# Performance work log

Hardware: AMD Instinct MI355X
Metric: run time of the kernel (lower is better)

## Reference

```python
import jax, jax.numpy as jnp
import numpy as np

S = 2048          # sequence length == max_seq_len
B = 256           # input_bits per token
H = 8             # num voting heads
NPER = 12         # RAM bits per neuron: min(similarity_bits, 12)
NPOS = 11         # relative-position bits: ceil(log2(max_seq_len))
SIM = 2 * B + NPOS  # similarity input bits = [query | key | rel_dist]
THRESH = H // 2   # threshold aggregation cutoff
MAXD = S - 1


def setup_inputs() -> dict:
    key = jax.random.key(0)
    k1, k2, k3 = jax.random.split(key, 3)
    tokens = jax.random.randint(k1, (S, B), 0, 2).astype(jnp.int32)      # bit tokens
    conn = jax.random.randint(k2, (H, NPER), 0, SIM).astype(jnp.int32)   # RAM wiring per head
    table = jax.random.randint(k3, (H, 2 ** NPER), 0, 2).astype(jnp.int32)  # RAM contents (0/1)
    return {"tokens": tokens, "conn": conn, "table": table}


def reference(tokens, conn, table):
    powers = (1 << jnp.arange(NPER)).astype(jnp.int32)            # address bit weights
    q_mask = (conn < B).astype(jnp.int32)
    k_mask = ((conn >= B) & (conn < 2 * B)).astype(jnp.int32)
    p_mask = (conn >= 2 * B).astype(jnp.int32)

    # Address decomposes additively over the three concat regions since wiring is fixed.
    tq = jnp.take(tokens, jnp.clip(conn, 0, B - 1), axis=1)        # [S,H,NPER]
    q_contrib = jnp.sum(tq * (q_mask * powers)[None], axis=-1)     # [S,H]
    tk = jnp.take(tokens, jnp.clip(conn - B, 0, B - 1), axis=1)
    k_contrib = jnp.sum(tk * (k_mask * powers)[None], axis=-1)     # [S,H]

    d = jnp.arange(S)
    rel_bits = ((d[:, None] >> jnp.arange(NPOS)[None, :]) & 1).astype(jnp.int32)  # [S,NPOS]
    tp = jnp.take(rel_bits, jnp.clip(conn - 2 * B, 0, NPOS - 1), axis=1)          # [S,H,NPER]
    p_contrib = jnp.sum(tp * (p_mask * powers)[None], axis=-1)     # [S,H] indexed by distance

    i = jnp.arange(S)
    dist = jnp.clip(i[:, None] - i[None, :], 0, MAXD)              # [S,S]
    addr = q_contrib[:, None, :] + k_contrib[None, :, :] + p_contrib[dist]  # [S,S,H]
    head_bits = table[jnp.arange(H)[None, None, :], addr]          # [S,S,H] RAM lookups

    causal = i[None, :] <= i[:, None]
    votes = jnp.where(causal, head_bits.sum(-1), 0)                # [S,S]

    # threshold aggregation: XOR (per-bit parity) of tokens with vote >= THRESH
    include = (votes >= THRESH).astype(jnp.int32)                  # [S,S]
    parity = jnp.einsum('ij,jb->ib', include, tokens) % 2          # [S,B]
    # fallback: first token achieving the max vote when nothing clears threshold
    fallback = tokens[jnp.argmax(votes, axis=1)]                   # [S,B]
    any_included = include.sum(axis=1, keepdims=True) > 0
    out = jnp.where(any_included, parity, fallback)
    return out.astype(jnp.uint8)
```

## Files before the change

kernel.cpp:

```cpp
#include <hip/hip_runtime.h>
#include <stdint.h>

#define S 2048
#define B 256
#define H 8
#define NPER 12
#define NPOS 11
#define THRESH 4

typedef unsigned long long u64;
typedef uint32_t u32;


__global__ void prep_kernel(const int* __restrict__ tokens,
                            const int* __restrict__ conn,
                            const int* __restrict__ table,
                            u64* __restrict__ packed_tokens,
                            uint16_t* __restrict__ qc,
                            uint16_t* __restrict__ kc,
                            uint16_t* __restrict__ pc,
                            u64* __restrict__ ptab) {
    const int bi = blockIdx.x;
    const int tid = threadIdx.x;

    if (bi >= S) {
        int k = (bi - S) * 256 + tid;
        int h = k >> 6, w = k & 63;
        const int* src = table + h * 4096 + w * 64;
        u64 v = 0;
        #pragma unroll 8
        for (int b = 0; b < 64; ++b) v |= (u64)(src[b] & 1) << b;
        ptab[k] = v;
        return;
    }

    __shared__ u64 srow[4];
    const int i = bi;
    const int lane = tid & 63, wave = tid >> 6;

    int t = tokens[i * B + tid];
    u64 m = __ballot(t != 0);
    if (lane == 0) {
        srow[wave] = m;
        packed_tokens[i * 4 + wave] = m;
    }
    __syncthreads();

    if (tid < H) {
        int h = tid;
        int q = 0, k = 0, p = 0;
        #pragma unroll
        for (int n = 0; n < NPER; ++n) {
            int c = conn[h * NPER + n];
            if (c < B) {
                q |= (int)((srow[c >> 6] >> (c & 63)) & 1) << n;
            } else if (c < 2 * B) {
                int cc = c - B;
                k |= (int)((srow[cc >> 6] >> (cc & 63)) & 1) << n;
            } else {
                int idx = c - 2 * B;
                p |= ((i >> idx) & 1) << n;
            }
        }
        qc[i * 8 + h] = (uint16_t)q;
        kc[i * 8 + h] = (uint16_t)k;
        pc[i * 8 + h] = (uint16_t)p;
    }
}

__launch_bounds__(256)
__global__ void main_kernel(const u64* __restrict__ packed_tokens,
                            const uint16_t* __restrict__ qc,
                            const uint16_t* __restrict__ kc,
                            const uint16_t* __restrict__ pc,
                            const u64* __restrict__ ptab,
                            int* __restrict__ out) {
    __shared__ u32 s_tab[1024];
    __shared__ u64 s_xor[4][4];
    __shared__ int s_key[4];
    __shared__ int s_any[4];

    const int tid = threadIdx.x;
    const int lane = tid & 63, wave = tid >> 6;

    ((uint4*)s_tab)[tid] = ((const uint4*)ptab)[tid];
    __syncthreads();

    auto do_row = [&](int i) {
        const u64* qv = (const u64*)(qc + i * 8);
        const u64 q0 = qv[0], q1 = qv[1];

        u64 x0 = 0, x1 = 0, x2 = 0, x3 = 0;
        int bestv = -1, bestj = 0, any = 0;

        const int niter = (i + 512) >> 9;
        for (int it = 0; it < niter; ++it) {
            const int ja = tid + (it << 9);
            const int jb = ja + 256;
            const int jca = min(ja, i), jcb = min(jb, i);
            const int da = i - jca, db = i - jcb;

            const ulonglong2 kA = *(const ulonglong2*)(kc + jca * 8);
            const ulonglong2 pA = *(const ulonglong2*)(pc + da * 8);
            const ulonglong2 kB = *(const ulonglong2*)(kc + jcb * 8);
            const ulonglong2 pB = *(const ulonglong2*)(pc + db * 8);
            const ulonglong2 tA0 = *(const ulonglong2*)(packed_tokens + jca * 4);
            const ulonglong2 tA1 = *(const ulonglong2*)(packed_tokens + jca * 4 + 2);
            const ulonglong2 tB0 = *(const ulonglong2*)(packed_tokens + jcb * 4);
            const ulonglong2 tB1 = *(const ulonglong2*)(packed_tokens + jcb * 4 + 2);

            const u64 aa0 = q0 + kA.x + pA.x, aa1 = q1 + kA.y + pA.y;
            const u64 ab0 = q0 + kB.x + pB.x, ab1 = q1 + kB.y + pB.y;

            int vA = 0, vB = 0;
            #pragma unroll
            for (int h = 0; h < 4; ++h) {
                { u32 w = (u32)(aa0 >> (16 * h + 5)) & 127;
                  vA += (int)((s_tab[h * 128 + w] >> ((u32)(aa0 >> (16 * h)) & 31)) & 1); }
                { u32 w = (u32)(aa1 >> (16 * h + 5)) & 127;
                  vA += (int)((s_tab[(h + 4) * 128 + w] >> ((u32)(aa1 >> (16 * h)) & 31)) & 1); }
                { u32 w = (u32)(ab0 >> (16 * h + 5)) & 127;
                  vB += (int)((s_tab[h * 128 + w] >> ((u32)(ab0 >> (16 * h)) & 31)) & 1); }
                { u32 w = (u32)(ab1 >> (16 * h + 5)) & 127;
                  vB += (int)((s_tab[(h + 4) * 128 + w] >> ((u32)(ab1 >> (16 * h)) & 31)) & 1); }
            }

            const bool actA = (ja <= i), actB = (jb <= i);
            const bool incA = actA && (vA >= THRESH);
            const bool incB = actB && (vB >= THRESH);
            const u64 mA = incA ? ~0ull : 0ull;
            const u64 mB = incB ? ~0ull : 0ull;
            x0 ^= (tA0.x & mA) ^ (tB0.x & mB);
            x1 ^= (tA0.y & mA) ^ (tB0.y & mB);
            x2 ^= (tA1.x & mA) ^ (tB1.x & mB);
            x3 ^= (tA1.y & mA) ^ (tB1.y & mB);
            any |= (int)incA | (int)incB;

            const int kvA = actA ? vA : -1;
            const int kvB = actB ? vB : -1;
            if (kvA > bestv) { bestv = kvA; bestj = ja; }
            if (kvB > bestv) { bestv = kvB; bestj = jb; }
        }

        int key = ((bestv + 1) << 16) | (2047 - bestj);
        u64 anym = __ballot(any != 0);
        #pragma unroll
        for (int off = 32; off > 0; off >>= 1) {
            key = max(key, __shfl_xor(key, off));
            x0 ^= __shfl_xor(x0, off);
            x1 ^= __shfl_xor(x1, off);
            x2 ^= __shfl_xor(x2, off);
            x3 ^= __shfl_xor(x3, off);
        }

        if (lane == 0) {
            s_xor[wave][0] = x0; s_xor[wave][1] = x1;
            s_xor[wave][2] = x2; s_xor[wave][3] = x3;
            s_key[wave] = key;
            s_any[wave] = (anym != 0ull) ? 1 : 0;
        }
        __syncthreads();

        const int fk = max(max(s_key[0], s_key[1]), max(s_key[2], s_key[3]));
        const int fa = s_any[0] | s_any[1] | s_any[2] | s_any[3];
        const int widx = tid >> 6, bitb = tid & 63;
        const u64 xw = s_xor[0][widx] ^ s_xor[1][widx] ^ s_xor[2][widx] ^ s_xor[3][widx];
        int o;
        if (fa) {
            o = (int)((xw >> bitb) & 1);
        } else {
            const int bj = 2047 - (fk & 0xFFFF);
            o = (int)((packed_tokens[bj * 4 + widx] >> bitb) & 1);
        }
        out[i * B + tid] = o;
        __syncthreads();
    };

    const int b = blockIdx.x;
    do_row(b);
    do_row(2047 - b);
}

extern "C" void kernel_launch(void* const* d_in, const int* in_sizes, int n_in,
                              void* d_out, int out_size, void* d_ws, size_t ws_size,
                              hipStream_t stream) {
    const int* tokens = (const int*)d_in[0];
    const int* conn   = (const int*)d_in[1];
    const int* table  = (const int*)d_in[2];
    int* out = (int*)d_out;

    uint8_t* ws = (uint8_t*)d_ws;
    u64* packed_tokens = (u64*)(ws);
    uint16_t* qc = (uint16_t*)(ws + 65536);
    uint16_t* kc = (uint16_t*)(ws + 98304);
    uint16_t* pc = (uint16_t*)(ws + 131072);
    u64* ptab    = (u64*)(ws + 163840);

    prep_kernel<<<S + 2, 256, 0, stream>>>(tokens, conn, table,
                                           packed_tokens, qc, kc, pc, ptab);
    main_kernel<<<S / 2, 256, 0, stream>>>(packed_tokens, qc, kc, pc, ptab, out);
}
```

Measured before the change: 22.03 us.

## Fuse paired short and long row processing into one loop sharing key and token loads

Each block handles row b and row 2047-b. Previously it did them one after the other. Now a single loop over the long row's keys also computes the short row whenever the iteration is in range, so the kc and packed-token loads are shared. The two rows' reductions are merged into one shuffle pass and one barrier. The 'any included' ballot is replaced by testing whether the best vote exceeds THRESH, and launch bounds now request 4 blocks per CU. The doubled accumulators raise register pressure, which could conflict with the occupancy hint.

```diff
diff --git a/kernel.cpp b/kernel.cpp
--- a/kernel.cpp
+++ b/kernel.cpp
@@ -68,7 +68,19 @@
     }
 }
 
-__launch_bounds__(256)
+__device__ __forceinline__ int vote8(const u32* s_tab, u64 a0, u64 a1) {
+    int v = 0;
+    #pragma unroll
+    for (int h = 0; h < 4; ++h) {
+        { u32 w = (u32)(a0 >> (16 * h + 5)) & 127;
+          v += (int)((s_tab[h * 128 + w] >> ((u32)(a0 >> (16 * h)) & 31)) & 1); }
+        { u32 w = (u32)(a1 >> (16 * h + 5)) & 127;
+          v += (int)((s_tab[(h + 4) * 128 + w] >> ((u32)(a1 >> (16 * h)) & 31)) & 1); }
+    }
+    return v;
+}
+
+__launch_bounds__(256, 4)
 __global__ void main_kernel(const u64* __restrict__ packed_tokens,
                             const uint16_t* __restrict__ qc,
                             const uint16_t* __restrict__ kc,
@@ -76,9 +88,7 @@
                             const u64* __restrict__ ptab,
                             int* __restrict__ out) {
     __shared__ u32 s_tab[1024];
-    __shared__ u64 s_xor[4][4];
-    __shared__ int s_key[4];
-    __shared__ int s_any[4];
+    __shared__ u64 s_red[4][9];
 
     const int tid = threadIdx.x;
     const int lane = tid & 63, wave = tid >> 6;
@@ -86,99 +96,115 @@
     ((uint4*)s_tab)[tid] = ((const uint4*)ptab)[tid];
     __syncthreads();
 
-    auto do_row = [&](int i) {
-        const u64* qv = (const u64*)(qc + i * 8);
-        const u64 q0 = qv[0], q1 = qv[1];
-
-        u64 x0 = 0, x1 = 0, x2 = 0, x3 = 0;
-        int bestv = -1, bestj = 0, any = 0;
-
-        const int niter = (i + 512) >> 9;
-        for (int it = 0; it < niter; ++it) {
-            const int ja = tid + (it << 9);
-            const int jb = ja + 256;
-            const int jca = min(ja, i), jcb = min(jb, i);
-            const int da = i - jca, db = i - jcb;
-
-            const ulonglong2 kA = *(const ulonglong2*)(kc + jca * 8);
-            const ulonglong2 pA = *(const ulonglong2*)(pc + da * 8);
-            const ulonglong2 kB = *(const ulonglong2*)(kc + jcb * 8);
-            const ulonglong2 pB = *(const ulonglong2*)(pc + db * 8);
-            const ulonglong2 tA0 = *(const ulonglong2*)(packed_tokens + jca * 4);
-            const ulonglong2 tA1 = *(const ulonglong2*)(packed_tokens + jca * 4 + 2);
-            const ulonglong2 tB0 = *(const ulonglong2*)(packed_tokens + jcb * 4);
-            const ulonglong2 tB1 = *(const ulonglong2*)(packed_tokens + jcb * 4 + 2);
-
-            const u64 aa0 = q0 + kA.x + pA.x, aa1 = q1 + kA.y + pA.y;
-            const u64 ab0 = q0 + kB.x + pB.x, ab1 = q1 + kB.y + pB.y;
-
-            int vA = 0, vB = 0;
-            #pragma unroll
-            for (int h = 0; h < 4; ++h) {
-                { u32 w = (u32)(aa0 >> (16 * h + 5)) & 127;
-                  vA += (int)((s_tab[h * 128 + w] >> ((u32)(aa0 >> (16 * h)) & 31)) & 1); }
-                { u32 w = (u32)(aa1 >> (16 * h + 5)) & 127;
-                  vA += (int)((s_tab[(h + 4) * 128 + w] >> ((u32)(aa1 >> (16 * h)) & 31)) & 1); }
-                { u32 w = (u32)(ab0 >> (16 * h + 5)) & 127;
-                  vB += (int)((s_tab[h * 128 + w] >> ((u32)(ab0 >> (16 * h)) & 31)) & 1); }
-                { u32 w = (u32)(ab1 >> (16 * h + 5)) & 127;
-                  vB += (int)((s_tab[(h + 4) * 128 + w] >> ((u32)(ab1 >> (16 * h)) & 31)) & 1); }
-            }
-
-            const bool actA = (ja <= i), actB = (jb <= i);
-            const bool incA = actA && (vA >= THRESH);
-            const bool incB = actB && (vB >= THRESH);
-            const u64 mA = incA ? ~0ull : 0ull;
-            const u64 mB = incB ? ~0ull : 0ull;
-            x0 ^= (tA0.x & mA) ^ (tB0.x & mB);
-            x1 ^= (tA0.y & mA) ^ (tB0.y & mB);
-            x2 ^= (tA1.x & mA) ^ (tB1.x & mB);
-            x3 ^= (tA1.y & mA) ^ (tB1.y & mB);
-            any |= (int)incA | (int)incB;
-
+    const int b  = blockIdx.x;
+    const int is = b;
+    const int ib = 2047 - b;
+
+    const u64* qvb = (const u64*)(qc + ib * 8);
+    const u64 qb0 = qvb[0], qb1 = qvb[1];
+    const u64* qvs = (const u64*)(qc + is * 8);
+    const u64 qs0 = qvs[0], qs1 = qvs[1];
+
+    u64 bx0 = 0, bx1 = 0, bx2 = 0, bx3 = 0;
+    u64 sx0 = 0, sx1 = 0, sx2 = 0, sx3 = 0;
+    int bbv = -1, bbj = 0, sbv = -1, sbj = 0;
+
+    const int niter = (ib + 512) >> 9;
+    for (int it = 0; it < niter; ++it) {
+        const int ja = tid + (it << 9);
+        const int jb = ja + 256;
+        const int jca = min(ja, ib), jcb = min(jb, ib);
+
+        const ulonglong2 kA  = *(const ulonglong2*)(kc + jca * 8);
+        const ulonglong2 kB  = *(const ulonglong2*)(kc + jcb * 8);
+        const ulonglong2 tA0 = *(const ulonglong2*)(packed_tokens + jca * 4);
+        const ulonglong2 tA1 = *(const ulonglong2*)(packed_tokens + jca * 4 + 2);
+        const ulonglong2 tB0 = *(const ulonglong2*)(packed_tokens + jcb * 4);
+        const ulonglong2 tB1 = *(const ulonglong2*)(packed_tokens + jcb * 4 + 2);
+
+        {
+            const ulonglong2 pA = *(const ulonglong2*)(pc + (ib - jca) * 8);
+            const ulonglong2 pB = *(const ulonglong2*)(pc + (ib - jcb) * 8);
+            const int vA = vote8(s_tab, qb0 + kA.x + pA.x, qb1 + kA.y + pA.y);
+            const int vB = vote8(s_tab, qb0 + kB.x + pB.x, qb1 + kB.y + pB.y);
+            const bool actA = (ja <= ib), actB = (jb <= ib);
+            const u64 mA = (actA && vA >= THRESH) ? ~0ull : 0ull;
+            const u64 mB = (actB && vB >= THRESH) ? ~0ull : 0ull;
+            bx0 ^= (tA0.x & mA) ^ (tB0.x & mB);
+            bx1 ^= (tA0.y & mA) ^ (tB0.y & mB);
+            bx2 ^= (tA1.x & mA) ^ (tB1.x & mB);
+            bx3 ^= (tA1.y & mA) ^ (tB1.y & mB);
             const int kvA = actA ? vA : -1;
             const int kvB = actB ? vB : -1;
-            if (kvA > bestv) { bestv = kvA; bestj = ja; }
-            if (kvB > bestv) { bestv = kvB; bestj = jb; }
+            if (kvA > bbv) { bbv = kvA; bbj = ja; }
+            if (kvB > bbv) { bbv = kvB; bbj = jb; }
         }
 
-        int key = ((bestv + 1) << 16) | (2047 - bestj);
-        u64 anym = __ballot(any != 0);
-        #pragma unroll
-        for (int off = 32; off > 0; off >>= 1) {
-            key = max(key, __shfl_xor(key, off));
-            x0 ^= __shfl_xor(x0, off);
-            x1 ^= __shfl_xor(x1, off);
-            x2 ^= __shfl_xor(x2, off);
-            x3 ^= __shfl_xor(x3, off);
+        if ((it << 9) <= is) {
+            const int jsa = min(ja, is), jsb = min(jb, is);
+            const ulonglong2 pA = *(const ulonglong2*)(pc + (is - jsa) * 8);
+            const ulonglong2 pB = *(const ulonglong2*)(pc + (is - jsb) * 8);
+            const int vA = vote8(s_tab, qs0 + kA.x + pA.x, qs1 + kA.y + pA.y);
+            const int vB = vote8(s_tab, qs0 + kB.x + pB.x, qs1 + kB.y + pB.y);
+            const bool actA = (ja <= is), actB = (jb <= is);
+            const u64 mA = (actA && vA >= THRESH) ? ~0ull : 0ull;
+            const u64 mB = (actB && vB >= THRESH) ? ~0ull : 0ull;
+            sx0 ^= (tA0.x & mA) ^ (tB0.x & mB);
+            sx1 ^= (tA0.y & mA) ^ (tB0.y & mB);
+            sx2 ^= (tA1.x & mA) ^ (tB1.x & mB);
+            sx3 ^= (tA1.y & mA) ^ (tB1.y & mB);
+            const int kvA = actA ? vA : -1;
+            const int kvB = actB ? vB : -1;
+            if (kvA > sbv) { sbv = kvA; sbj = ja; }
+            if (kvB > sbv) { sbv = kvB; sbj = jb; }
         }
-
-        if (lane == 0) {
-            s_xor[wave][0] = x0; s_xor[wave][1] = x1;
-            s_xor[wave][2] = x2; s_xor[wave][3] = x3;
-            s_key[wave] = key;
-            s_any[wave] = (anym != 0ull) ? 1 : 0;
-        }
-        __syncthreads();
-
-        const int fk = max(max(s_key[0], s_key[1]), max(s_key[2], s_key[3]));
-        const int fa = s_any[0] | s_any[1] | s_any[2] | s_any[3];
-        const int widx = tid >> 6, bitb = tid & 63;
-        const u64 xw = s_xor[0][widx] ^ s_xor[1][widx] ^ s_xor[2][widx] ^ s_xor[3][widx];
-        int o;
-        if (fa) {
-            o = (int)((xw >> bitb) & 1);
-        } else {
-            const int bj = 2047 - (fk & 0xFFFF);
-            o = (int)((packed_tokens[bj * 4 + widx] >> bitb) & 1);
-        }
-        out[i * B + tid] = o;
-        __syncthreads();
-    };
-
-    const int b = blockIdx.x;
-    do_row(b);
-    do_row(2047 - b);
+    }
+
+    u32 bkey = (u32)(((bbv + 1) << 16) | (2047 - bbj));
+    u32 skey = (u32)(((sbv + 1) << 16) | (2047 - sbj));
+
+    #pragma unroll
+    for (int off = 32; off > 0; off >>= 1) {
+        bkey = max(bkey, (u32)__shfl_xor((int)bkey, off));
+        skey = max(skey, (u32)__shfl_xor((int)skey, off));
+        bx0 ^= __shfl_xor(bx0, off); bx1 ^= __shfl_xor(bx1, off);
+        bx2 ^= __shfl_xor(bx2, off); bx3 ^= __shfl_xor(bx3, off);
+        sx0 ^= __shfl_xor(sx0, off); sx1 ^= __shfl_xor(sx1, off);
+        sx2 ^= __shfl_xor(sx2, off); sx3 ^= __shfl_xor(sx3, off);
+    }
+
+    if (lane == 0) {
+        s_red[wave][0] = bx0; s_red[wave][1] = bx1;
+        s_red[wave][2] = bx2; s_red[wave][3] = bx3;
+        s_red[wave][4] = sx0; s_red[wave][5] = sx1;
+        s_red[wave][6] = sx2; s_red[wave][7] = sx3;
+        s_red[wave][8] = ((u64)bkey << 32) | skey;
+    }
+    __syncthreads();
+
+    const int widx = tid >> 6, bitb = tid & 63;
+    u64 xwb = s_red[0][widx]     ^ s_red[1][widx]     ^ s_red[2][widx]     ^ s_red[3][widx];
+    u64 xws = s_red[0][4 + widx] ^ s_red[1][4 + widx] ^ s_red[2][4 + widx] ^ s_red[3][4 + widx];
+    u64 kk0 = s_red[0][8], kk1 = s_red[1][8], kk2 = s_red[2][8], kk3 = s_red[3][8];
+    const u32 fkb = max(max((u32)(kk0 >> 32), (u32)(kk1 >> 32)),
+                        max((u32)(kk2 >> 32), (u32)(kk3 >> 32)));
+    const u32 fks = max(max((u32)kk0, (u32)kk1), max((u32)kk2, (u32)kk3));
+
+    int ob, os;
+    if ((fkb >> 16) > THRESH) {
+        ob = (int)((xwb >> bitb) & 1);
+    } else {
+        const int bj = 2047 - (int)(fkb & 0xFFFF);
+        ob = (int)((packed_tokens[bj * 4 + widx] >> bitb) & 1);
+    }
+    if ((fks >> 16) > THRESH) {
+        os = (int)((xws >> bitb) & 1);
+    } else {
+        const int bj = 2047 - (int)(fks & 0xFFFF);
+        os = (int)((packed_tokens[bj * 4 + widx] >> bitb) & 1);
+    }
+    out[ib * B + tid] = ob;
+    out[is * B + tid] = os;
 }
 
 extern "C" void kernel_launch(void* const* d_in, const int* in_sizes, int n_in,
```

Measured after the change: 22.45 us. About the same (+1.9%).
